# Kernel tuning notes

Measured on AMD Instinct MI355X. Metric: run time of the kernel, lower is better.

## Reference

```python
import jax, jax.numpy as jnp
import numpy as np

N, E, G = 100000, 3200000, 256
IN_C, HID = 3, 32


def setup_inputs() -> dict:
    key = jax.random.key(0)
    ks = jax.random.split(key, 10)
    x = jax.random.normal(ks[0], (N, IN_C), dtype=jnp.float32)
    edge_index = jax.random.randint(ks[1], (2, E), 0, N, dtype=jnp.int64)
    edge_weight = jax.random.uniform(ks[2], (E,), dtype=jnp.float32)
    batch = jnp.sort(jax.random.randint(ks[3], (N,), 0, G, dtype=jnp.int64))
    # GCNConv params (PyG: out = norm-agg(x @ W) + b), glorot-ish init
    W0 = jax.random.normal(ks[4], (IN_C, HID), dtype=jnp.float32) / np.sqrt(IN_C)
    b0 = jnp.zeros((HID,), dtype=jnp.float32)
    W1 = jax.random.normal(ks[5], (HID, HID), dtype=jnp.float32) / np.sqrt(HID)
    b1 = jnp.zeros((HID,), dtype=jnp.float32)
    Wr = jax.random.normal(ks[6], (HID, 1), dtype=jnp.float32) / np.sqrt(HID)
    br = jnp.zeros((1,), dtype=jnp.float32)
    return {"x": x, "edge_index": edge_index, "edge_weight": edge_weight,
            "batch": batch, "W0": W0, "b0": b0, "W1": W1, "b1": b1,
            "Wr": Wr, "br": br}


def _gcn_conv(x, row, col, w_edge, W, b, n_nodes):
    # PyG GCNConv with add_self_loops + symmetric normalization
    h = x @ W                                   # [N, H]
    deg = jax.ops.segment_sum(w_edge, col, num_segments=n_nodes)
    dinv = jnp.where(deg > 0, jax.lax.rsqrt(deg), 0.0)
    norm = dinv[row] * w_edge * dinv[col]       # [E+N]
    msg = h[row] * norm[:, None]                # gather + scale
    agg = jax.ops.segment_sum(msg, col, num_segments=n_nodes)
    return agg + b


def reference(x, edge_index, edge_weight, batch, W0, b0, W1, b1, Wr, br):
    n = x.shape[0]
    loop = jnp.arange(n, dtype=edge_index.dtype)
    row = jnp.concatenate([edge_index[0], loop])   # source (j)
    col = jnp.concatenate([edge_index[1], loop])   # target (i)
    w = jnp.concatenate([edge_weight, jnp.ones((n,), dtype=edge_weight.dtype)])

    h = jax.nn.relu(_gcn_conv(x, row, col, w, W0, b0, n))
    h = jax.nn.relu(_gcn_conv(h, row, col, w, W1, b1, n))

    # global_mean_pool over graphs
    ones = jnp.ones((n,), dtype=h.dtype)
    cnt = jax.ops.segment_sum(ones, batch, num_segments=G)
    summed = jax.ops.segment_sum(h, batch, num_segments=G)
    hg = summed / jnp.maximum(cnt, 1.0)[:, None]   # [G, H]
    return (hg @ Wr + br).squeeze(-1)              # [G]
```

## Files before the change

kernel.cpp:

```cpp
#include <hip/hip_runtime.h>
#include <hip/hip_fp16.h>


#define TPB 256
#define NBMAX 512
#define BSH 8
#define BSZ 256
#define CAP 9216
#define ST 1024
#define SV 16
#define STILE (ST * SV)

typedef unsigned long long u64;
union H8 { float4 f4; __half2 h2[4]; };
union H4 { u64 u; __half2 h2[2]; };
union HU { __half h; unsigned short u; };

__global__ void k_init(unsigned* cursor, float* gsum, float* gcnt, int nb, int g) {
    int t = threadIdx.x;
    for (int j = t; j < nb; j += blockDim.x) cursor[j] = 0u;
    for (int j = t; j < g; j += blockDim.x) { gsum[j] = 0.0f; gcnt[j] = 0.0f; }
}

__global__ void __launch_bounds__(1024) k_scat(const int* __restrict__ row,
                       const int* __restrict__ col, const float* __restrict__ w,
                       unsigned* cursor, int2* __restrict__ tmp, int nb, int e) {
    __shared__ unsigned cl[NBMAX];
    __shared__ unsigned bl[NBMAX];
    int t = threadIdx.x;
    for (int j = t; j < nb; j += ST) cl[j] = 0u;
    __syncthreads();
    const int4* c4 = (const int4*)col;
    int e4 = e >> 2;
    int base4 = blockIdx.x * (STILE >> 2);
    int4 cv[SV / 4];
    unsigned rk[SV];
    bool vld[SV / 4];
    #pragma unroll
    for (int v = 0; v < SV / 4; ++v) {
        int i4 = base4 + t + v * ST;
        vld[v] = (i4 < e4);
        if (vld[v]) {
            cv[v] = c4[i4];
            rk[4 * v + 0] = atomicAdd(&cl[cv[v].x >> BSH], 1u);
            rk[4 * v + 1] = atomicAdd(&cl[cv[v].y >> BSH], 1u);
            rk[4 * v + 2] = atomicAdd(&cl[cv[v].z >> BSH], 1u);
            rk[4 * v + 3] = atomicAdd(&cl[cv[v].w >> BSH], 1u);
        }
    }
    int tailc = -1; unsigned tailrk = 0; int taili = 0;
    if (blockIdx.x == 0) {
        int i = (e4 << 2) + t;
        if (i < e) { taili = i; tailc = col[i]; tailrk = atomicAdd(&cl[tailc >> BSH], 1u); }
    }
    __syncthreads();
    for (int j = t; j < nb; j += ST) {
        unsigned c = cl[j];
        bl[j] = c ? atomicAdd(&cursor[j], c) : 0u;
    }
    __syncthreads();
    const int4* r4 = (const int4*)row;
    const float4* w4 = (const float4*)w;
    #pragma unroll
    for (int v = 0; v < SV / 4; ++v) {
        if (vld[v]) {
            int i4 = base4 + t + v * ST;
            int4 rr = r4[i4];
            float4 ww = w4[i4];
            int c, b; unsigned lo;
            c = cv[v].x; b = c >> BSH; lo = bl[b] + rk[4 * v + 0];
            if (lo < CAP) tmp[(size_t)b * CAP + lo] =
                make_int2((int)(((unsigned)(c & 255) << 24) | (unsigned)rr.x), __float_as_int(ww.x));
            c = cv[v].y; b = c >> BSH; lo = bl[b] + rk[4 * v + 1];
            if (lo < CAP) tmp[(size_t)b * CAP + lo] =
                make_int2((int)(((unsigned)(c & 255) << 24) | (unsigned)rr.y), __float_as_int(ww.y));
            c = cv[v].z; b = c >> BSH; lo = bl[b] + rk[4 * v + 2];
            if (lo < CAP) tmp[(size_t)b * CAP + lo] =
                make_int2((int)(((unsigned)(c & 255) << 24) | (unsigned)rr.z), __float_as_int(ww.z));
            c = cv[v].w; b = c >> BSH; lo = bl[b] + rk[4 * v + 3];
            if (lo < CAP) tmp[(size_t)b * CAP + lo] =
                make_int2((int)(((unsigned)(c & 255) << 24) | (unsigned)rr.w), __float_as_int(ww.w));
        }
    }
    if (tailc >= 0) {
        int b = tailc >> BSH; unsigned lo = bl[b] + tailrk;
        if (lo < CAP) tmp[(size_t)b * CAP + lo] =
            make_int2((int)(((unsigned)(tailc & 255) << 24) | (unsigned)row[taili]),
                      __float_as_int(w[taili]));
    }
}

__global__ void __launch_bounds__(1024) k_conv(const int2* __restrict__ tmp,
                       const unsigned* __restrict__ cursor, unsigned* __restrict__ nodeinfo,
                       float* __restrict__ dinv, unsigned* __restrict__ arr, int n) {
    __shared__ unsigned cnt[BSZ];
    __shared__ float dw[BSZ];
    __shared__ unsigned cur[BSZ];
    int t = threadIdx.x, b = blockIdx.x;
    if (t < BSZ) { cnt[t] = 0u; dw[t] = 1.0f; }
    __syncthreads();
    unsigned cb = cursor[b]; if (cb > CAP) cb = CAP;
    size_t base = (size_t)b * CAP;
    for (unsigned k = t; k < cb; k += 1024) {
        int2 p = tmp[base + k];
        unsigned c = (unsigned)p.x >> 24;
        atomicAdd(&cnt[c], 1u);
        atomicAdd(&dw[c], __int_as_float(p.y));
    }
    __syncthreads();
    unsigned v = 0;
    if (t < BSZ) { v = cnt[t]; cur[t] = v; }
    __syncthreads();
    for (int off = 1; off < BSZ; off <<= 1) {
        unsigned u = (t < BSZ && t >= off) ? cur[t - off] : 0u;
        __syncthreads();
        if (t < BSZ) cur[t] += u;
        __syncthreads();
    }
    if (t < BSZ) {
        unsigned excl = cur[t] - v;
        int node = (b << BSH) + t;
        if (node < n) {
            unsigned cc = v > 1023u ? 1023u : v;
            nodeinfo[node] = (cc << 22) | (unsigned)(base + excl);
            dinv[node] = rsqrtf(dw[t]);
        }
        cur[t] = excl;
    }
    __syncthreads();
    for (unsigned k = t; k < cb; k += 1024) {
        int2 p = tmp[base + k];
        unsigned c = (unsigned)p.x >> 24;
        unsigned slot = atomicAdd(&cur[c], 1u);
        HU wu; wu.h = __float2half(__int_as_float(p.y));
        arr[base + slot] = ((unsigned)(wu.u & 0x7FFFu) << 17) | ((unsigned)p.x & 0x1FFFFu);
    }
}

__global__ void k_xw0(const float* __restrict__ x, const float* __restrict__ W0,
                      const float* __restrict__ dinv, float4* __restrict__ hw4, int n) {
    int t = blockIdx.x * blockDim.x + threadIdx.x;
    if (t >= n * 4) return;
    int i = t >> 2, q = t & 3;
    float x0 = x[i * 3 + 0], x1 = x[i * 3 + 1], x2 = x[i * 3 + 2];
    float di = dinv[i];
    int cb = q * 8;
    H8 u;
    #pragma unroll
    for (int j = 0; j < 4; ++j) {
        int c = cb + 2 * j;
        float a = di * (x0 * W0[c]     + x1 * W0[32 + c]     + x2 * W0[64 + c]);
        float b = di * (x0 * W0[c + 1] + x1 * W0[32 + c + 1] + x2 * W0[64 + c + 1]);
        u.h2[j] = __float22half2_rn(make_float2(a, b));
    }
    hw4[t] = u.f4;
}

#define EDGE_ACC(V) { \
    unsigned rr = (V) & 0x1FFFFu; \
    HU wu; wu.u = (unsigned short)((V) >> 17); \
    float wv = __half2float(wu.h); \
    H4 g; g.u = hw8[(rr << 3) + q]; \
    float2 f0 = __half22float2(g.h2[0]); \
    float2 f1 = __half22float2(g.h2[1]); \
    a0.x = fmaf(wv, f0.x, a0.x); a0.y = fmaf(wv, f0.y, a0.y); \
    a1.x = fmaf(wv, f1.x, a1.x); a1.y = fmaf(wv, f1.y, a1.y); }

__global__ void __launch_bounds__(256) k_agg1(const u64* __restrict__ hw8,
                      const unsigned* __restrict__ arr, const unsigned* __restrict__ nodeinfo,
                      const float* __restrict__ dinv, const float* __restrict__ W1,
                      const float* __restrict__ b0, u64* __restrict__ out8, int n) {
    __shared__ float W1s[1024];
    __shared__ float hl[32][33];
    int tid = threadIdx.x;
    for (int j = tid; j < 1024; j += 256) W1s[j] = W1[j];
    int t = blockIdx.x * 256 + tid;
    int i = t >> 3, q = t & 7;
    if (i >= n) i = n - 1;
    int li = tid >> 3;
    unsigned info = nodeinfo[i];
    unsigned k = info & 0x3FFFFFu;
    unsigned hi = k + (info >> 22);
    int idx = (i << 3) + q;
    H4 s; s.u = hw8[idx];
    float2 a0 = __half22float2(s.h2[0]);
    float2 a1 = __half22float2(s.h2[1]);
    for (; k + 8 <= hi; k += 8) {
        unsigned v0 = __builtin_nontemporal_load(arr + k + 0);
        unsigned v1 = __builtin_nontemporal_load(arr + k + 1);
        unsigned v2 = __builtin_nontemporal_load(arr + k + 2);
        unsigned v3 = __builtin_nontemporal_load(arr + k + 3);
        unsigned v4 = __builtin_nontemporal_load(arr + k + 4);
        unsigned v5 = __builtin_nontemporal_load(arr + k + 5);
        unsigned v6 = __builtin_nontemporal_load(arr + k + 6);
        unsigned v7 = __builtin_nontemporal_load(arr + k + 7);
        EDGE_ACC(v0) EDGE_ACC(v1) EDGE_ACC(v2) EDGE_ACC(v3)
        EDGE_ACC(v4) EDGE_ACC(v5) EDGE_ACC(v6) EDGE_ACC(v7)
    }
    for (; k < hi; ++k) {
        unsigned v = __builtin_nontemporal_load(arr + k);
        EDGE_ACC(v)
    }
    float di = dinv[i];
    int cb = q << 2;
    hl[li][cb + 0] = fmaxf(di * a0.x + b0[cb + 0], 0.0f);
    hl[li][cb + 1] = fmaxf(di * a0.y + b0[cb + 1], 0.0f);
    hl[li][cb + 2] = fmaxf(di * a1.x + b0[cb + 2], 0.0f);
    hl[li][cb + 3] = fmaxf(di * a1.y + b0[cb + 3], 0.0f);
    __syncthreads();
    float o0 = 0.0f, o1 = 0.0f, o2 = 0.0f, o3 = 0.0f;
    #pragma unroll
    for (int kk = 0; kk < 32; ++kk) {
        float hv = hl[li][kk];
        const float* wr = &W1s[(kk << 5) + cb];
        o0 = fmaf(hv, wr[0], o0);
        o1 = fmaf(hv, wr[1], o1);
        o2 = fmaf(hv, wr[2], o2);
        o3 = fmaf(hv, wr[3], o3);
    }
    H4 oh;
    oh.h2[0] = __float22half2_rn(make_float2(di * o0, di * o1));
    oh.h2[1] = __float22half2_rn(make_float2(di * o2, di * o3));
    out8[idx] = oh.u;
}

__global__ void __launch_bounds__(256) k_agg2(const u64* __restrict__ hw8,
                      const unsigned* __restrict__ arr, const unsigned* __restrict__ nodeinfo,
                      const float* __restrict__ dinv, const float* __restrict__ b1,
                      const float* __restrict__ Wr, const int* __restrict__ batch,
                      float* gsum, float* gcnt, int n) {
    int t = blockIdx.x * 256 + threadIdx.x;
    int i = t >> 3, q = t & 7;
    bool active = (i < n);
    int ii = active ? i : (n - 1);
    unsigned info = active ? nodeinfo[ii] : 0u;
    unsigned k = info & 0x3FFFFFu;
    unsigned hi = k + (info >> 22);
    int idx = (ii << 3) + q;
    H4 s; s.u = hw8[idx];
    float2 a0 = __half22float2(s.h2[0]);
    float2 a1 = __half22float2(s.h2[1]);
    for (; k + 8 <= hi; k += 8) {
        unsigned v0 = __builtin_nontemporal_load(arr + k + 0);
        unsigned v1 = __builtin_nontemporal_load(arr + k + 1);
        unsigned v2 = __builtin_nontemporal_load(arr + k + 2);
        unsigned v3 = __builtin_nontemporal_load(arr + k + 3);
        unsigned v4 = __builtin_nontemporal_load(arr + k + 4);
        unsigned v5 = __builtin_nontemporal_load(arr + k + 5);
        unsigned v6 = __builtin_nontemporal_load(arr + k + 6);
        unsigned v7 = __builtin_nontemporal_load(arr + k + 7);
        EDGE_ACC(v0) EDGE_ACC(v1) EDGE_ACC(v2) EDGE_ACC(v3)
        EDGE_ACC(v4) EDGE_ACC(v5) EDGE_ACC(v6) EDGE_ACC(v7)
    }
    for (; k < hi; ++k) {
        unsigned v = __builtin_nontemporal_load(arr + k);
        EDGE_ACC(v)
    }
    float di = dinv[ii];
    int cb = q << 2;
    float sp = 0.0f;
    sp = fmaf(fmaxf(di * a0.x + b1[cb + 0], 0.0f), Wr[cb + 0], sp);
    sp = fmaf(fmaxf(di * a0.y + b1[cb + 1], 0.0f), Wr[cb + 1], sp);
    sp = fmaf(fmaxf(di * a1.x + b1[cb + 2], 0.0f), Wr[cb + 2], sp);
    sp = fmaf(fmaxf(di * a1.y + b1[cb + 3], 0.0f), Wr[cb + 3], sp);
    if (!active) sp = 0.0f;
    sp += __shfl_xor(sp, 1);
    sp += __shfl_xor(sp, 2);
    sp += __shfl_xor(sp, 4);
    int b = active ? batch[ii] : -1;
    int b0v = __shfl(b, 0, 64);
    bool uniform = (b0v >= 0) && (__ballot(b == b0v) == 0xFFFFFFFFFFFFFFFFULL);
    if (uniform) {
        float tot = sp;
        tot += __shfl_xor(tot, 8);
        tot += __shfl_xor(tot, 16);
        tot += __shfl_xor(tot, 32);
        if ((threadIdx.x & 63) == 0) {
            atomicAdd(&gsum[b0v], tot);
            atomicAdd(&gcnt[b0v], 8.0f);
        }
    } else if (active && q == 0) {
        atomicAdd(&gsum[b], sp);
        atomicAdd(&gcnt[b], 1.0f);
    }
}

__global__ void k_final(const float* gsum, const float* gcnt, const float* __restrict__ br,
                        float* out, int g) {
    int i = blockIdx.x * blockDim.x + threadIdx.x;
    if (i < g) out[i] = gsum[i] / fmaxf(gcnt[i], 1.0f) + br[0];
}

extern "C" void kernel_launch(void* const* d_in, const int* in_sizes, int n_in,
                              void* d_out, int out_size, void* d_ws, size_t ws_size,
                              hipStream_t stream) {
    const float* x     = (const float*)d_in[0];
    const int*   ei    = (const int*)d_in[1];
    const float* ew    = (const float*)d_in[2];
    const int*   batch = (const int*)d_in[3];
    const float* W0    = (const float*)d_in[4];
    const float* b0    = (const float*)d_in[5];
    const float* W1    = (const float*)d_in[6];
    const float* b1    = (const float*)d_in[7];
    const float* Wr    = (const float*)d_in[8];
    const float* br    = (const float*)d_in[9];
    float* out = (float*)d_out;

    int n = in_sizes[0] / 3;
    int e = in_sizes[2];
    int g = out_size;
    const int* row = ei;
    const int* col = ei + e;
    int nb = (n + BSZ - 1) >> BSH;

    char* ws = (char*)d_ws;
    size_t off = 0;
    auto alloc = [&](size_t bytes) -> void* {
        void* p = ws + off;
        off += (bytes + 255) & ~(size_t)255;
        return p;
    };
    unsigned* cursor   = (unsigned*)alloc((size_t)NBMAX * 4);
    unsigned* nodeinfo = (unsigned*)alloc((size_t)n * 4);
    float*    dinv     = (float*)   alloc((size_t)n * 4);
    float*    gsum     = (float*)   alloc((size_t)g * 4);
    float*    gcnt     = (float*)   alloc((size_t)g * 4);
    unsigned* arr      = (unsigned*)alloc((size_t)nb * CAP * 4);
    char*     region   = (char*)    alloc((size_t)nb * CAP * 8);
    int2*   tmp  = (int2*)region;
    __half* hWh1 = (__half*)region;
    __half* hWh2 = (__half*)(region + (size_t)n * 64);
    (void)ws_size;

    int stiles = (e + STILE - 1) / STILE;
    int nq4    = (n * 4 + TPB - 1) / TPB;
    int nq8    = (n * 8 + TPB - 1) / TPB;

    k_init  <<<1,      1024, 0, stream>>>(cursor, gsum, gcnt, nb, g);
    k_scat  <<<stiles, ST,   0, stream>>>(row, col, ew, cursor, tmp, nb, e);
    k_conv  <<<nb,     1024, 0, stream>>>(tmp, cursor, nodeinfo, dinv, arr, n);
    k_xw0   <<<nq4,    TPB,  0, stream>>>(x, W0, dinv, (float4*)hWh1, n);
    k_agg1  <<<nq8,    TPB,  0, stream>>>((const u64*)hWh1, arr, nodeinfo, dinv, W1, b0, (u64*)hWh2, n);
    k_agg2  <<<nq8,    TPB,  0, stream>>>((const u64*)hWh2, arr, nodeinfo, dinv, b1, Wr, batch, gsum, gcnt, n);
    k_final <<<1,      TPB,  0, stream>>>(gsum, gcnt, br, out, g);
}
```

Before: 284.6 us.

## Process each node with 2 threads of 16 channels instead of 8 threads of 4

The two aggregation kernels now assign two threads per node, each gathering 32 bytes (two float4) of fp16 features per edge, where before eight threads each loaded 8 bytes. Edge-list index loads are issued by a quarter as many threads, so each thread does more work per edge and the per-edge index traffic is amortized. Biases and the readout weights are staged in shared memory, and the pooling reduction is adjusted to match. The cost is more registers per thread, lower thread-level parallelism, more load imbalance across nodes of different degree, and less coalesced wide gathers.

```diff
diff --git a/kernel.cpp b/kernel.cpp
--- a/kernel.cpp
+++ b/kernel.cpp
@@ -13,7 +13,6 @@
 
 typedef unsigned long long u64;
 union H8 { float4 f4; __half2 h2[4]; };
-union H4 { u64 u; __half2 h2[2]; };
 union HU { __half h; unsigned short u; };
 
 __global__ void k_init(unsigned* cursor, float* gsum, float* gcnt, int nb, int g) {
@@ -156,132 +155,153 @@
     hw4[t] = u.f4;
 }
 
-#define EDGE_ACC(V) { \
-    unsigned rr = (V) & 0x1FFFFu; \
-    HU wu; wu.u = (unsigned short)((V) >> 17); \
-    float wv = __half2float(wu.h); \
-    H4 g; g.u = hw8[(rr << 3) + q]; \
-    float2 f0 = __half22float2(g.h2[0]); \
-    float2 f1 = __half22float2(g.h2[1]); \
-    a0.x = fmaf(wv, f0.x, a0.x); a0.y = fmaf(wv, f0.y, a0.y); \
-    a1.x = fmaf(wv, f1.x, a1.x); a1.y = fmaf(wv, f1.y, a1.y); }
-
-__global__ void __launch_bounds__(256) k_agg1(const u64* __restrict__ hw8,
-                      const unsigned* __restrict__ arr, const unsigned* __restrict__ nodeinfo,
-                      const float* __restrict__ dinv, const float* __restrict__ W1,
-                      const float* __restrict__ b0, u64* __restrict__ out8, int n) {
+#define EACC(V) { \
+    unsigned rr_ = (V) & 0x1FFFFu; \
+    HU wu_; wu_.u = (unsigned short)((V) >> 17); \
+    float wv_ = __half2float(wu_.h); \
+    H8 gA_, gB_; \
+    gA_.f4 = tb[(size_t)rr_ << 2]; \
+    gB_.f4 = tb[((size_t)rr_ << 2) + 1]; \
+    float2 f_; \
+    f_ = __half22float2(gA_.h2[0]); a[0] = fmaf(wv_, f_.x, a[0]); a[1] = fmaf(wv_, f_.y, a[1]); \
+    f_ = __half22float2(gA_.h2[1]); a[2] = fmaf(wv_, f_.x, a[2]); a[3] = fmaf(wv_, f_.y, a[3]); \
+    f_ = __half22float2(gA_.h2[2]); a[4] = fmaf(wv_, f_.x, a[4]); a[5] = fmaf(wv_, f_.y, a[5]); \
+    f_ = __half22float2(gA_.h2[3]); a[6] = fmaf(wv_, f_.x, a[6]); a[7] = fmaf(wv_, f_.y, a[7]); \
+    f_ = __half22float2(gB_.h2[0]); a[8] = fmaf(wv_, f_.x, a[8]); a[9] = fmaf(wv_, f_.y, a[9]); \
+    f_ = __half22float2(gB_.h2[1]); a[10]= fmaf(wv_, f_.x, a[10]);a[11]= fmaf(wv_, f_.y, a[11]);\
+    f_ = __half22float2(gB_.h2[2]); a[12]= fmaf(wv_, f_.x, a[12]);a[13]= fmaf(wv_, f_.y, a[13]);\
+    f_ = __half22float2(gB_.h2[3]); a[14]= fmaf(wv_, f_.x, a[14]);a[15]= fmaf(wv_, f_.y, a[15]);}
+
+#define EDGE_LOOP() { \
+    for (; k + 4 <= hi; k += 4) { \
+        unsigned v0 = __builtin_nontemporal_load(arr + k + 0); \
+        unsigned v1 = __builtin_nontemporal_load(arr + k + 1); \
+        unsigned v2 = __builtin_nontemporal_load(arr + k + 2); \
+        unsigned v3 = __builtin_nontemporal_load(arr + k + 3); \
+        EACC(v0) EACC(v1) EACC(v2) EACC(v3) \
+    } \
+    for (; k < hi; ++k) { \
+        unsigned v = __builtin_nontemporal_load(arr + k); \
+        EACC(v) \
+    } }
+
+__global__ void __launch_bounds__(256) k_agg1(const float4* __restrict__ tab4,
+        const unsigned* __restrict__ arr, const unsigned* __restrict__ nodeinfo,
+        const float* __restrict__ dinv, const float* __restrict__ W1,
+        const float* __restrict__ b0, float4* __restrict__ out4, int n) {
     __shared__ float W1s[1024];
-    __shared__ float hl[32][33];
+    __shared__ float b0s[32];
+    __shared__ float hl[128 * 33];
     int tid = threadIdx.x;
     for (int j = tid; j < 1024; j += 256) W1s[j] = W1[j];
+    if (tid < 32) b0s[tid] = b0[tid];
     int t = blockIdx.x * 256 + tid;
-    int i = t >> 3, q = t & 7;
+    int i = t >> 1, q = t & 1;
     if (i >= n) i = n - 1;
-    int li = tid >> 3;
+    int li = tid >> 1;
     unsigned info = nodeinfo[i];
     unsigned k = info & 0x3FFFFFu;
     unsigned hi = k + (info >> 22);
-    int idx = (i << 3) + q;
-    H4 s; s.u = hw8[idx];
-    float2 a0 = __half22float2(s.h2[0]);
-    float2 a1 = __half22float2(s.h2[1]);
-    for (; k + 8 <= hi; k += 8) {
-        unsigned v0 = __builtin_nontemporal_load(arr + k + 0);
-        unsigned v1 = __builtin_nontemporal_load(arr + k + 1);
-        unsigned v2 = __builtin_nontemporal_load(arr + k + 2);
-        unsigned v3 = __builtin_nontemporal_load(arr + k + 3);
-        unsigned v4 = __builtin_nontemporal_load(arr + k + 4);
-        unsigned v5 = __builtin_nontemporal_load(arr + k + 5);
-        unsigned v6 = __builtin_nontemporal_load(arr + k + 6);
-        unsigned v7 = __builtin_nontemporal_load(arr + k + 7);
-        EDGE_ACC(v0) EDGE_ACC(v1) EDGE_ACC(v2) EDGE_ACC(v3)
-        EDGE_ACC(v4) EDGE_ACC(v5) EDGE_ACC(v6) EDGE_ACC(v7)
-    }
-    for (; k < hi; ++k) {
-        unsigned v = __builtin_nontemporal_load(arr + k);
-        EDGE_ACC(v)
-    }
+    const float4* tb = tab4 + (q << 1);
+    float a[16];
+    {
+        H8 sA, sB;
+        sA.f4 = tb[(size_t)i << 2];
+        sB.f4 = tb[((size_t)i << 2) + 1];
+        #pragma unroll
+        for (int j = 0; j < 4; ++j) {
+            float2 f0 = __half22float2(sA.h2[j]);
+            float2 f1 = __half22float2(sB.h2[j]);
+            a[2*j] = f0.x; a[2*j+1] = f0.y;
+            a[8+2*j] = f1.x; a[8+2*j+1] = f1.y;
+        }
+    }
+    EDGE_LOOP()
     float di = dinv[i];
-    int cb = q << 2;
-    hl[li][cb + 0] = fmaxf(di * a0.x + b0[cb + 0], 0.0f);
-    hl[li][cb + 1] = fmaxf(di * a0.y + b0[cb + 1], 0.0f);
-    hl[li][cb + 2] = fmaxf(di * a1.x + b0[cb + 2], 0.0f);
-    hl[li][cb + 3] = fmaxf(di * a1.y + b0[cb + 3], 0.0f);
-    __syncthreads();
-    float o0 = 0.0f, o1 = 0.0f, o2 = 0.0f, o3 = 0.0f;
+    int cb = q << 4;
+    float* hr = hl + li * 33;
+    #pragma unroll
+    for (int j = 0; j < 16; ++j)
+        hr[cb + j] = fmaxf(di * a[j] + b0s[cb + j], 0.0f);
+    __syncthreads();
+    float o[16];
+    #pragma unroll
+    for (int j = 0; j < 16; ++j) o[j] = 0.0f;
     #pragma unroll
     for (int kk = 0; kk < 32; ++kk) {
-        float hv = hl[li][kk];
-        const float* wr = &W1s[(kk << 5) + cb];
-        o0 = fmaf(hv, wr[0], o0);
-        o1 = fmaf(hv, wr[1], o1);
-        o2 = fmaf(hv, wr[2], o2);
-        o3 = fmaf(hv, wr[3], o3);
-    }
-    H4 oh;
-    oh.h2[0] = __float22half2_rn(make_float2(di * o0, di * o1));
-    oh.h2[1] = __float22half2_rn(make_float2(di * o2, di * o3));
-    out8[idx] = oh.u;
-}
-
-__global__ void __launch_bounds__(256) k_agg2(const u64* __restrict__ hw8,
-                      const unsigned* __restrict__ arr, const unsigned* __restrict__ nodeinfo,
-                      const float* __restrict__ dinv, const float* __restrict__ b1,
-                      const float* __restrict__ Wr, const int* __restrict__ batch,
-                      float* gsum, float* gcnt, int n) {
-    int t = blockIdx.x * 256 + threadIdx.x;
-    int i = t >> 3, q = t & 7;
+        float hv = hr[kk];
+        const float* wr = W1s + (kk << 5) + cb;
+        #pragma unroll
+        for (int j = 0; j < 16; ++j) o[j] = fmaf(hv, wr[j], o[j]);
+    }
+    H8 oA, oB;
+    #pragma unroll
+    for (int j = 0; j < 4; ++j) {
+        oA.h2[j] = __float22half2_rn(make_float2(di * o[2*j],     di * o[2*j+1]));
+        oB.h2[j] = __float22half2_rn(make_float2(di * o[8+2*j],   di * o[8+2*j+1]));
+    }
+    out4[((size_t)i << 2) + (q << 1)]     = oA.f4;
+    out4[((size_t)i << 2) + (q << 1) + 1] = oB.f4;
+}
+
+__global__ void __launch_bounds__(256) k_agg2(const float4* __restrict__ tab4,
+        const unsigned* __restrict__ arr, const unsigned* __restrict__ nodeinfo,
+        const float* __restrict__ dinv, const float* __restrict__ b1,
+        const float* __restrict__ Wr, const int* __restrict__ batch,
+        float* gsum, float* gcnt, int n) {
+    __shared__ float b1s[32];
+    __shared__ float Wrs[32];
+    int tid = threadIdx.x;
+    if (tid < 32) { b1s[tid] = b1[tid]; Wrs[tid] = Wr[tid]; }
+    __syncthreads();
+    int t = blockIdx.x * 256 + tid;
+    int i = t >> 1, q = t & 1;
     bool active = (i < n);
     int ii = active ? i : (n - 1);
     unsigned info = active ? nodeinfo[ii] : 0u;
     unsigned k = info & 0x3FFFFFu;
     unsigned hi = k + (info >> 22);
-    int idx = (ii << 3) + q;
-    H4 s; s.u = hw8[idx];
-    float2 a0 = __half22float2(s.h2[0]);
-    float2 a1 = __half22float2(s.h2[1]);
-    for (; k + 8 <= hi; k += 8) {
-        unsigned v0 = __builtin_nontemporal_load(arr + k + 0);
-        unsigned v1 = __builtin_nontemporal_load(arr + k + 1);
-        unsigned v2 = __builtin_nontemporal_load(arr + k + 2);
-        unsigned v3 = __builtin_nontemporal_load(arr + k + 3);
-        unsigned v4 = __builtin_nontemporal_load(arr + k + 4);
-        unsigned v5 = __builtin_nontemporal_load(arr + k + 5);
-        unsigned v6 = __builtin_nontemporal_load(arr + k + 6);
-        unsigned v7 = __builtin_nontemporal_load(arr + k + 7);
-        EDGE_ACC(v0) EDGE_ACC(v1) EDGE_ACC(v2) EDGE_ACC(v3)
-        EDGE_ACC(v4) EDGE_ACC(v5) EDGE_ACC(v6) EDGE_ACC(v7)
-    }
-    for (; k < hi; ++k) {
-        unsigned v = __builtin_nontemporal_load(arr + k);
-        EDGE_ACC(v)
-    }
+    const float4* tb = tab4 + (q << 1);
+    float a[16];
+    {
+        H8 sA, sB;
+        sA.f4 = tb[(size_t)ii << 2];
+        sB.f4 = tb[((size_t)ii << 2) + 1];
+        #pragma unroll
+        for (int j = 0; j < 4; ++j) {
+            float2 f0 = __half22float2(sA.h2[j]);
+            float2 f1 = __half22float2(sB.h2[j]);
+            a[2*j] = f0.x; a[2*j+1] = f0.y;
+            a[8+2*j] = f1.x; a[8+2*j+1] = f1.y;
+        }
+    }
+    EDGE_LOOP()
     float di = dinv[ii];
-    int cb = q << 2;
+    int cb = q << 4;
     float sp = 0.0f;
-    sp = fmaf(fmaxf(di * a0.x + b1[cb + 0], 0.0f), Wr[cb + 0], sp);
-    sp = fmaf(fmaxf(di * a0.y + b1[cb + 1], 0.0f), Wr[cb + 1], sp);
-    sp = fmaf(fmaxf(di * a1.x + b1[cb + 2], 0.0f), Wr[cb + 2], sp);
-    sp = fmaf(fmaxf(di * a1.y + b1[cb + 3], 0.0f), Wr[cb + 3], sp);
+    #pragma unroll
+    for (int j = 0; j < 16; ++j)
+        sp = fmaf(fmaxf(di * a[j] + b1s[cb + j], 0.0f), Wrs[cb + j], sp);
     if (!active) sp = 0.0f;
     sp += __shfl_xor(sp, 1);
-    sp += __shfl_xor(sp, 2);
-    sp += __shfl_xor(sp, 4);
-    int b = active ? batch[ii] : -1;
-    int b0v = __shfl(b, 0, 64);
-    bool uniform = (b0v >= 0) && (__ballot(b == b0v) == 0xFFFFFFFFFFFFFFFFULL);
+    int bb = active ? batch[ii] : -1;
+    int b0v = __shfl(bb, 0, 64);
+    bool uniform = (b0v >= 0) && (__ballot(bb == b0v) == 0xFFFFFFFFFFFFFFFFULL);
     if (uniform) {
-        float tot = sp;
+        float tot = (q == 0) ? sp : 0.0f;
+        tot += __shfl_xor(tot, 1);
+        tot += __shfl_xor(tot, 2);
+        tot += __shfl_xor(tot, 4);
         tot += __shfl_xor(tot, 8);
         tot += __shfl_xor(tot, 16);
         tot += __shfl_xor(tot, 32);
-        if ((threadIdx.x & 63) == 0) {
+        if ((tid & 63) == 0) {
             atomicAdd(&gsum[b0v], tot);
-            atomicAdd(&gcnt[b0v], 8.0f);
+            atomicAdd(&gcnt[b0v], 32.0f);
         }
     } else if (active && q == 0) {
-        atomicAdd(&gsum[b], sp);
-        atomicAdd(&gcnt[b], 1.0f);
+        atomicAdd(&gsum[bb], sp);
+        atomicAdd(&gcnt[bb], 1.0f);
     }
 }
 
@@ -328,19 +348,19 @@
     unsigned* arr      = (unsigned*)alloc((size_t)nb * CAP * 4);
     char*     region   = (char*)    alloc((size_t)nb * CAP * 8);
     int2*   tmp  = (int2*)region;
-    __half* hWh1 = (__half*)region;
-    __half* hWh2 = (__half*)(region + (size_t)n * 64);
+    float4* tab1 = (float4*)region;
+    float4* tab2 = (float4*)(region + (size_t)n * 64);
     (void)ws_size;
 
     int stiles = (e + STILE - 1) / STILE;
     int nq4    = (n * 4 + TPB - 1) / TPB;
-    int nq8    = (n * 8 + TPB - 1) / TPB;
+    int nq2    = (n * 2 + TPB - 1) / TPB;
 
     k_init  <<<1,      1024, 0, stream>>>(cursor, gsum, gcnt, nb, g);
     k_scat  <<<stiles, ST,   0, stream>>>(row, col, ew, cursor, tmp, nb, e);
     k_conv  <<<nb,     1024, 0, stream>>>(tmp, cursor, nodeinfo, dinv, arr, n);
-    k_xw0   <<<nq4,    TPB,  0, stream>>>(x, W0, dinv, (float4*)hWh1, n);
-    k_agg1  <<<nq8,    TPB,  0, stream>>>((const u64*)hWh1, arr, nodeinfo, dinv, W1, b0, (u64*)hWh2, n);
-    k_agg2  <<<nq8,    TPB,  0, stream>>>((const u64*)hWh2, arr, nodeinfo, dinv, b1, Wr, batch, gsum, gcnt, n);
+    k_xw0   <<<nq4,    TPB,  0, stream>>>(x, W0, dinv, tab1, n);
+    k_agg1  <<<nq2,    TPB,  0, stream>>>(tab1, arr, nodeinfo, dinv, W1, b0, tab2, n);
+    k_agg2  <<<nq2,    TPB,  0, stream>>>(tab2, arr, nodeinfo, dinv, b1, Wr, batch, gsum, gcnt, n);
     k_final <<<1,      TPB,  0, stream>>>(gsum, gcnt, br, out, g);
 }
```

After: 288.2 us. No clear change (+1.3%).
